# Performance work log

Measured on AMD Instinct MI355X. Metric: run time of the kernel, lower is better.

## Reference

```python
import jax, jax.numpy as jnp
import numpy as np

B, S, D = 1, 2048, 2048
H, G, HD = 32, 8, 64          # heads, kv groups, head_dim
GS = H // G                   # group size = 4
EPS = 1e-6


def _rmsnorm(v, w):
    vf = v.astype(jnp.float32)
    n = vf * jax.lax.rsqrt(jnp.mean(vf * vf, axis=-1, keepdims=True) + EPS)
    return (n * (1.0 + w.astype(jnp.float32))).astype(v.dtype)


def _rope(v, cos, sin):
    # v: [b, h, s, hd]; cos/sin: [s, hd] (rot_dim == head_dim)
    half = v.shape[-1] // 2
    x1, x2 = v[..., :half], v[..., half:]
    rotated = jnp.concatenate([-x2, x1], axis=-1)
    c = cos[None, None, :, :]
    s = sin[None, None, :, :]
    return (v * c + rotated * s).astype(v.dtype)


def setup_inputs() -> dict:
    key = jax.random.key(0)
    ks = jax.random.split(key, 8)
    x = jax.random.normal(ks[0], (B, S, D), dtype=jnp.float32)
    # causal mask: True above diagonal => masked out
    mask = jnp.triu(jnp.ones((S, S), dtype=bool), k=1)
    # standard RoPE tables, full rotary dim == head_dim
    inv_freq = 1.0 / (10000.0 ** (jnp.arange(0, HD, 2, dtype=jnp.float32) / HD))
    angles = jnp.arange(S, dtype=jnp.float32)[:, None] * inv_freq[None, :]
    angles = jnp.concatenate([angles, angles], axis=-1)  # [S, HD]
    cos = jnp.cos(angles)
    sin = jnp.sin(angles)
    sc = 1.0 / np.sqrt(D)
    Wq = jax.random.normal(ks[1], (2 * H * HD, D), dtype=jnp.float32) * sc
    Wk = jax.random.normal(ks[2], (G * HD, D), dtype=jnp.float32) * sc
    Wv = jax.random.normal(ks[3], (G * HD, D), dtype=jnp.float32) * sc
    Wo = jax.random.normal(ks[4], (D, H * HD), dtype=jnp.float32) * sc
    q_norm_w = jnp.zeros((HD,), dtype=jnp.float32)
    k_norm_w = jnp.zeros((HD,), dtype=jnp.float32)
    return {"x": x, "mask": mask, "cos": cos, "sin": sin, "Wq": Wq,
            "Wk": Wk, "Wv": Wv, "Wo": Wo,
            "q_norm_w": q_norm_w, "k_norm_w": k_norm_w}


def reference(x, mask, cos, sin, Wq, Wk, Wv, Wo, q_norm_w, k_norm_w):
    b, s, _ = x.shape
    d_out = H * HD
    # fused q + gate projection: [b, s, H, 2*HD]
    qg = jnp.einsum('bsd,ed->bse', x, Wq).reshape(b, s, H, 2 * HD)
    q = qg[..., :HD]                         # [b, s, H, HD]
    gate = qg[..., HD:].reshape(b, s, d_out)  # [b, s, d_out]
    k = jnp.einsum('bsd,ed->bse', x, Wk).reshape(b, s, G, HD)
    v = jnp.einsum('bsd,ed->bse', x, Wv).reshape(b, s, G, HD)
    q = q.transpose(0, 2, 1, 3)   # [b, H, s, HD]
    k = k.transpose(0, 2, 1, 3)   # [b, G, s, HD]
    v = v.transpose(0, 2, 1, 3)
    q = _rmsnorm(q, q_norm_w)
    k = _rmsnorm(k, k_norm_w)
    q = _rope(q, cos[:s], sin[:s])
    k = _rope(k, cos[:s], sin[:s])
    # GQA without materializing repeated K/V: group queries as [b, G, GS, s, HD]
    qg_ = q.reshape(b, G, GS, s, HD)
    scores = jnp.einsum('bghqd,bgkd->bghqk', qg_, k)   # [b, G, GS, s, s]
    scores = jnp.where(mask[None, None, None, :s, :s], -jnp.inf, scores)
    scale = HD ** (-0.5)
    w = jax.nn.softmax((scores * scale).astype(jnp.float32), axis=-1).astype(q.dtype)
    ctx = jnp.einsum('bghqk,bgkd->bghqd', w, v)        # [b, G, GS, s, HD]
    ctx = ctx.reshape(b, H, s, HD).transpose(0, 2, 1, 3).reshape(b, s, d_out)
    ctx = ctx * jax.nn.sigmoid(gate)
    return jnp.einsum('bse,de->bsd', ctx, Wo)
```

## Files before the change

kernel.cpp:

```cpp
#include <hip/hip_runtime.h>

typedef __bf16 bf16;
typedef __bf16 bf16x4 __attribute__((ext_vector_type(4)));
typedef __bf16 bf16x8 __attribute__((ext_vector_type(8)));
typedef float f32x4 __attribute__((ext_vector_type(4)));

#define DEV static __device__ __forceinline__

constexpr int S  = 2048;
constexpr int D  = 2048;
constexpr int H  = 32;
constexpr int G  = 8;
constexpr int HD = 64;
constexpr int NQG = 2 * H * HD;
constexpr int LDP = 72;

DEV bf16x8 load8(const bf16* p) { return *reinterpret_cast<const bf16x8*>(p); }

DEV f32x4 mfma16(bf16x8 a, bf16x8 b, f32x4 c) {
  return __builtin_amdgcn_mfma_f32_16x16x32_bf16(a, b, c, 0, 0, 0);
}

DEV void gload_lds16(const bf16* g, bf16* l) {
  __builtin_amdgcn_global_load_lds(
      (const __attribute__((address_space(1))) void*)g,
      (__attribute__((address_space(3))) void*)l, 16, 0, 0);
}

#define BARRIER() asm volatile("s_barrier" ::: "memory")
#define VMDRAIN() asm volatile("s_waitcnt vmcnt(0)" ::: "memory")

template <int NISS>
DEV void stage_tile(bf16* lds, const bf16* src_row0, size_t ld, int k0, int tid) {
  const int w = tid >> 6, l = tid & 63;
#pragma unroll
  for (int i = 0; i < NISS; ++i) {
    int blk = w * NISS + i;
    int r = blk * 8 + (l >> 3);
    int c = (l & 7) ^ (r & 7);
    gload_lds16(src_row0 + (size_t)r * ld + k0 + c * 8, lds + blk * 512);
  }
}

DEV void stage64_8w(bf16* lds, const bf16* src_row0, size_t ld, int k0, int tid) {
  const int w = tid >> 6, l = tid & 63;
  int r = w * 8 + (l >> 3);
  int c = (l & 7) ^ (r & 7);
  gload_lds16(src_row0 + (size_t)r * ld + k0 + c * 8, lds + w * 512);
}

DEV bf16x8 fragr(const bf16* T, int row, int chunk) {
  return load8(T + row * 64 + (((chunk ^ (row & 7)) << 3)));
}

DEV float fexp2(float x) { return __builtin_amdgcn_exp2f(x); }
DEV float frcp(float x)  { return __builtin_amdgcn_rcpf(x); }

__global__ __launch_bounds__(256) void cvt_all(
    const float* __restrict__ x,  const float* __restrict__ wq,
    const float* __restrict__ wk, const float* __restrict__ wv,
    const float* __restrict__ wo,
    bf16* __restrict__ xb,  bf16* __restrict__ wqb, bf16* __restrict__ wkb,
    bf16* __restrict__ wvb, bf16* __restrict__ wob)
{
  long c = (long)blockIdx.x * 256 + threadIdx.x;
  const float* src; bf16* dst; long off;
  if      (c <  524288) { src = x;  dst = xb;  off = c; }
  else if (c < 1572864) { src = wq; dst = wqb; off = c -  524288; }
  else if (c < 1703936) { src = wk; dst = wkb; off = c - 1572864; }
  else if (c < 1835008) { src = wv; dst = wvb; off = c - 1703936; }
  else                  { src = wo; dst = wob; off = c - 1835008; }
  long i = off * 8;
  const float4* p = reinterpret_cast<const float4*>(src + i);
  float4 a = p[0], b = p[1];
  bf16x8 o;
  o[0] = (bf16)a.x; o[1] = (bf16)a.y; o[2] = (bf16)a.z; o[3] = (bf16)a.w;
  o[4] = (bf16)b.x; o[5] = (bf16)b.y; o[6] = (bf16)b.z; o[7] = (bf16)b.w;
  *reinterpret_cast<bf16x8*>(dst + i) = o;
}

DEV void rms_rope_store(f32x4 acc[4][4], bf16* __restrict__ dst,
                        const float* __restrict__ w,
                        const float* __restrict__ cosb,
                        const float* __restrict__ sinb,
                        int s0, int ln, int hi, float outscale)
{
  float wgt[4];
#pragma unroll
  for (int ni = 0; ni < 4; ++ni) wgt[ni] = 1.0f + w[ni * 16 + ln];
#pragma unroll
  for (int mi = 0; mi < 4; ++mi)
#pragma unroll
    for (int j = 0; j < 4; ++j) {
      int s = s0 + mi * 16 + hi * 4 + j;
      float v0 = acc[mi][0][j], v1 = acc[mi][1][j];
      float v2 = acc[mi][2][j], v3 = acc[mi][3][j];
      float ss = v0 * v0 + v1 * v1 + v2 * v2 + v3 * v3;
      ss += __shfl_xor(ss, 1);
      ss += __shfl_xor(ss, 2);
      ss += __shfl_xor(ss, 4);
      ss += __shfl_xor(ss, 8);
      float inv = __builtin_amdgcn_rsqf(ss * (1.0f / 64.0f) + 1e-6f);
      float xf[4] = {v0 * inv * wgt[0], v1 * inv * wgt[1],
                     v2 * inv * wgt[2], v3 * inv * wgt[3]};
#pragma unroll
      for (int ni = 0; ni < 4; ++ni) {
        int d = ni * 16 + ln;
        float c  = cosb[s * HD + d];
        float sn = sinb[s * HD + d];
        float rot = (ni < 2) ? -xf[ni + 2] : xf[ni - 2];
        dst[(size_t)s * HD + d] = (bf16)((xf[ni] * c + rot * sn) * outscale);
      }
    }
}

__global__ __launch_bounds__(256, 3) void gemm_qkv(
    const bf16* __restrict__ X, const bf16* __restrict__ Wq,
    const bf16* __restrict__ Wk, const bf16* __restrict__ Wv,
    const float* __restrict__ cosb, const float* __restrict__ sinb,
    const float* __restrict__ qw, const float* __restrict__ kw,
    bf16* __restrict__ qg, bf16* __restrict__ qrot,
    bf16* __restrict__ krot, bf16* __restrict__ vt)
{
  __shared__ __align__(16) bf16 As[128 * 64];
  __shared__ __align__(16) bf16 Bs[128 * 64];

  const int tid  = threadIdx.x;
  const int wave = tid >> 6;
  const int lane = tid & 63;
  const int ln = lane & 15, hi = lane >> 4;
  const int wm = wave >> 1, wn = wave & 1;
  const int m0 = blockIdx.y * 128;
  const int nt = blockIdx.x;

  const bf16* W; int n0;
  if (nt < 32)      { W = Wq; n0 = nt * 128; }
  else if (nt < 36) { W = Wk; n0 = (nt - 32) * 128; }
  else              { W = Wv; n0 = (nt - 36) * 128; }

  const bf16* arow = X + (size_t)m0 * D;
  const bf16* brow = W + (size_t)n0 * D;

  f32x4 acc[4][4] = {};

  for (int k0 = 0; k0 < D; k0 += 64) {
    __syncthreads();
    stage_tile<4>(As, arow, D, k0, tid);
    stage_tile<4>(Bs, brow, D, k0, tid);
    __syncthreads();
#pragma unroll
    for (int kk = 0; kk < 64; kk += 32) {
      bf16x8 a[4], b[4];
#pragma unroll
      for (int mi = 0; mi < 4; ++mi) a[mi] = fragr(As, wm * 64 + mi * 16 + ln, (kk >> 3) + hi);
#pragma unroll
      for (int ni = 0; ni < 4; ++ni) b[ni] = fragr(Bs, wn * 64 + ni * 16 + ln, (kk >> 3) + hi);
#pragma unroll
      for (int mi = 0; mi < 4; ++mi)
#pragma unroll
        for (int ni = 0; ni < 4; ++ni)
          acc[mi][ni] = mfma16(a[mi], b[ni], acc[mi][ni]);
    }
  }

  const int s0 = m0 + wm * 64;
  if (nt < 32) {
    if (wn == 0) {
      rms_rope_store(acc, qrot + (size_t)nt * S * HD, qw, cosb, sinb,
                     s0, ln, hi, 0.18033688011111204f);
    } else {
#pragma unroll
      for (int mi = 0; mi < 4; ++mi)
#pragma unroll
        for (int ni = 0; ni < 4; ++ni)
#pragma unroll
          for (int j = 0; j < 4; ++j) {
            int r = s0 + mi * 16 + hi * 4 + j;
            int c = nt * 128 + 64 + ni * 16 + ln;
            qg[(size_t)r * NQG + c] = (bf16)acc[mi][ni][j];
          }
    }
  } else if (nt < 36) {
    int g8 = (nt - 32) * 2 + wn;
    rms_rope_store(acc, krot + (size_t)g8 * S * HD, kw, cosb, sinb,
                   s0, ln, hi, 1.0f);
  } else {
    int nrel = (nt - 36) * 128;
#pragma unroll
    for (int mi = 0; mi < 4; ++mi)
#pragma unroll
      for (int ni = 0; ni < 4; ++ni)
#pragma unroll
        for (int j = 0; j < 4; ++j) {
          int r = s0 + mi * 16 + hi * 4 + j;
          int c = nrel + wn * 64 + ni * 16 + ln;
          vt[(size_t)c * S + r] = (bf16)acc[mi][ni][j];
        }
  }
}

__global__ __launch_bounds__(256, 3) void gemm_out(
    const bf16* __restrict__ A, const bf16* __restrict__ W,
    float* __restrict__ C)
{
  __shared__ __align__(16) bf16 As[128 * 64];
  __shared__ __align__(16) bf16 Bs[64 * 64];

  const int tid  = threadIdx.x;
  const int wave = tid >> 6;
  const int lane = tid & 63;
  const int ln = lane & 15, hi = lane >> 4;
  const int m0 = blockIdx.y * 128;
  const int n0 = blockIdx.x * 64;

  const bf16* arow = A + (size_t)m0 * D;
  const bf16* brow = W + (size_t)n0 * D;

  f32x4 acc[2][4] = {};

  for (int k0 = 0; k0 < D; k0 += 64) {
    __syncthreads();
    stage_tile<4>(As, arow, D, k0, tid);
    stage_tile<2>(Bs, brow, D, k0, tid);
    __syncthreads();
#pragma unroll
    for (int kk = 0; kk < 64; kk += 32) {
      bf16x8 a[2], b[4];
#pragma unroll
      for (int mi = 0; mi < 2; ++mi) a[mi] = fragr(As, wave * 32 + mi * 16 + ln, (kk >> 3) + hi);
#pragma unroll
      for (int ni = 0; ni < 4; ++ni) b[ni] = fragr(Bs, ni * 16 + ln, (kk >> 3) + hi);
#pragma unroll
      for (int mi = 0; mi < 2; ++mi)
#pragma unroll
        for (int ni = 0; ni < 4; ++ni)
          acc[mi][ni] = mfma16(a[mi], b[ni], acc[mi][ni]);
    }
  }

#pragma unroll
  for (int mi = 0; mi < 2; ++mi)
#pragma unroll
    for (int ni = 0; ni < 4; ++ni)
#pragma unroll
      for (int j = 0; j < 4; ++j) {
        int r = m0 + wave * 32 + mi * 16 + hi * 4 + j;
        int c = n0 + ni * 16 + ln;
        C[(size_t)r * D + c] = acc[mi][ni][j];
      }
}

DEV void attn_phase(const bf16* __restrict__ qrot, const bf16* __restrict__ krow,
                    const bf16* __restrict__ vrow, const bf16* __restrict__ qg,
                    bf16* __restrict__ ctxg,
                    bf16* Kb0, bf16* Kb1, bf16* Vb0, bf16* Vb1, bf16* pw,
                    int h, int qchunk, int nt, int ln, int hi, int tid)
{
  const int qb = qchunk * 64 + ((tid >> 6) & 3) * 16;
  const int q  = qb + ln;

  const bf16* qbase = qrot + ((size_t)h * S + qb + ln) * HD + hi * 8;
  bf16x8 q0 = load8(qbase);
  bf16x8 q1 = load8(qbase + 32);

  f32x4 po[4] = {};
  float m = -INFINITY, l = 0.f;

  stage64_8w(Kb0, krow, 64, 0, tid);
  stage64_8w(Vb0, vrow, S, 0, tid);
  VMDRAIN();
  BARRIER();

  int cur = 0;
  for (int t = 0; t < nt; ++t) {
    const bf16* Kb = cur ? Kb1 : Kb0;
    const bf16* Vb = cur ? Vb1 : Vb0;

    if (t + 1 < nt) {
      bf16* Kn = cur ? Kb0 : Kb1;
      bf16* Vn = cur ? Vb0 : Vb1;
      stage64_8w(Kn, krow + (size_t)(t + 1) * 64 * 64, 64, 0, tid);
      stage64_8w(Vn, vrow, S, (t + 1) * 64, tid);
    }

    bf16x8 kf0[4], kf1[4];
#pragma unroll
    for (int kr = 0; kr < 4; ++kr) {
      kf0[kr] = fragr(Kb, kr * 16 + ln, hi);
      kf1[kr] = fragr(Kb, kr * 16 + ln, hi + 4);
    }
    bf16x8 bv0[4], bv1[4];
#pragma unroll
    for (int dt = 0; dt < 4; ++dt) {
      bv0[dt] = fragr(Vb, dt * 16 + ln, hi);
      bv1[dt] = fragr(Vb, dt * 16 + ln, hi + 4);
    }

    f32x4 sc[4] = {};
    __builtin_amdgcn_s_setprio(1);
#pragma unroll
    for (int kr = 0; kr < 4; ++kr) {
      sc[kr] = mfma16(kf0[kr], q0, sc[kr]);
      sc[kr] = mfma16(kf1[kr], q1, sc[kr]);
    }
    __builtin_amdgcn_s_setprio(0);

    float pmax = -INFINITY;
    if (t == nt - 1) {
      const int key0 = t << 6;
#pragma unroll
      for (int kr = 0; kr < 4; ++kr)
#pragma unroll
        for (int j = 0; j < 4; ++j) {
          int key = key0 + kr * 16 + hi * 4 + j;
          float v = (key <= q) ? sc[kr][j] : -INFINITY;
          sc[kr][j] = v;
          pmax = fmaxf(pmax, v);
        }
    } else {
#pragma unroll
      for (int kr = 0; kr < 4; ++kr)
#pragma unroll
        for (int j = 0; j < 4; ++j) pmax = fmaxf(pmax, sc[kr][j]);
    }
    pmax = fmaxf(pmax, __shfl_xor(pmax, 16));
    pmax = fmaxf(pmax, __shfl_xor(pmax, 32));

    if (__any(pmax > m + 8.0f)) {
      float mn = fmaxf(m, pmax);
      float c  = fexp2(m - mn);
      l *= c;
      float cc[4];
#pragma unroll
      for (int j = 0; j < 4; ++j) cc[j] = __shfl(c, hi * 4 + j);
#pragma unroll
      for (int dt = 0; dt < 4; ++dt)
#pragma unroll
        for (int j = 0; j < 4; ++j) po[dt][j] *= cc[j];
      m = mn;
    }

    float ps = 0.f;
#pragma unroll
    for (int kr = 0; kr < 4; ++kr)
#pragma unroll
      for (int j = 0; j < 4; ++j) {
        float e = fexp2(sc[kr][j] - m);
        sc[kr][j] = e;
        ps += e;
      }
    ps += __shfl_xor(ps, 16);
    ps += __shfl_xor(ps, 32);
    l += ps;

#pragma unroll
    for (int kr = 0; kr < 4; ++kr) {
      unsigned w0, w1;
      asm("v_cvt_pk_bf16_f32 %0, %1, %2" : "=v"(w0) : "v"(sc[kr][0]), "v"(sc[kr][1]));
      asm("v_cvt_pk_bf16_f32 %0, %1, %2" : "=v"(w1) : "v"(sc[kr][2]), "v"(sc[kr][3]));
      uint2 w = {w0, w1};
      *reinterpret_cast<uint2*>(pw + ln * LDP + kr * 16 + hi * 4) = w;
    }
    bf16x8 pa0 = load8(pw + ln * LDP + hi * 8);
    bf16x8 pa1 = load8(pw + ln * LDP + 32 + hi * 8);

    __builtin_amdgcn_s_setprio(1);
#pragma unroll
    for (int dt = 0; dt < 4; ++dt) {
      po[dt] = mfma16(pa0, bv0[dt], po[dt]);
      po[dt] = mfma16(pa1, bv1[dt], po[dt]);
    }
    __builtin_amdgcn_s_setprio(0);

    VMDRAIN();
    BARRIER();
    cur ^= 1;
  }

  float lf[4];
#pragma unroll
  for (int j = 0; j < 4; ++j) lf[j] = __shfl(l, hi * 4 + j);
#pragma unroll
  for (int dt = 0; dt < 4; ++dt)
#pragma unroll
    for (int j = 0; j < 4; ++j) {
      int qq = qb + hi * 4 + j;
      int d  = dt * 16 + ln;
      float o  = po[dt][j] * frcp(lf[j]);
      float gv = (float)qg[(size_t)qq * NQG + h * 128 + 64 + d];
      float sg = frcp(1.0f + fexp2(gv * -1.442695040888963f));
      ctxg[(size_t)qq * D + h * 64 + d] = (bf16)(o * sg);
    }
}

__global__ __launch_bounds__(512) void attn(
    const bf16* __restrict__ qrot, const bf16* __restrict__ krot,
    const bf16* __restrict__ vt, const bf16* __restrict__ qg,
    bf16* __restrict__ ctxg)
{
  __shared__ __align__(16) bf16 Kbuf[2][64 * 64];
  __shared__ __align__(16) bf16 Vbuf[2][64 * 64];
  __shared__ __align__(16) bf16 Pl[8][16 * LDP];

  const int tid  = threadIdx.x;
  const int lane = tid & 63;
  const int ln = lane & 15, hi = lane >> 4;

  const int bid = blockIdx.x;
  const int g   = bid & 7;
  const int i   = bid >> 3;
  const int hp  = i & 1;
  const int pr  = i >> 1;
  const int h   = g * 4 + hp * 2 + ((tid >> 6) >> 2);
  bf16* pw = &Pl[tid >> 6][0];

  const bf16* krow = krot + (size_t)g * S * HD;
  const bf16* vrow = vt + (size_t)g * 64 * S;

  attn_phase(qrot, krow, vrow, qg, ctxg,
             &Kbuf[0][0], &Kbuf[1][0], &Vbuf[0][0], &Vbuf[1][0], pw,
             h, pr, pr + 1, ln, hi, tid);
  attn_phase(qrot, krow, vrow, qg, ctxg,
             &Kbuf[0][0], &Kbuf[1][0], &Vbuf[0][0], &Vbuf[1][0], pw,
             h, 31 - pr, 32 - pr, ln, hi, tid);
}

extern "C" void kernel_launch(void* const* d_in, const int* in_sizes, int n_in,
                              void* d_out, int out_size, void* d_ws, size_t ws_size,
                              hipStream_t stream) {
  const float* x    = (const float*)d_in[0];
  const float* cosb = (const float*)d_in[2];
  const float* sinb = (const float*)d_in[3];
  const float* Wq   = (const float*)d_in[4];
  const float* Wk   = (const float*)d_in[5];
  const float* Wv   = (const float*)d_in[6];
  const float* Wo   = (const float*)d_in[7];
  const float* qw   = (const float*)d_in[8];
  const float* kw   = (const float*)d_in[9];

  char* ws = (char*)d_ws;
  bf16* xb   = (bf16*)(ws);
  bf16* Wqb  = (bf16*)(ws + ( 8u << 20));
  bf16* Wkb  = (bf16*)(ws + (24u << 20));
  bf16* Wvb  = (bf16*)(ws + (26u << 20));
  bf16* Wob  = (bf16*)(ws + (28u << 20));
  bf16* qg   = (bf16*)(ws + (36u << 20));
  bf16* vt   = (bf16*)(ws + (54u << 20));
  bf16* qrot = (bf16*)(ws + (56u << 20));
  bf16* krot = (bf16*)(ws + (64u << 20));
  bf16* ctxg = (bf16*)(ws + (66u << 20));
  float* out = (float*)d_out;

  cvt_all<<<dim3(9216), 256, 0, stream>>>(x, Wq, Wk, Wv, Wo,
                                          xb, Wqb, Wkb, Wvb, Wob);

  gemm_qkv<<<dim3(40, 16), 256, 0, stream>>>(xb, Wqb, Wkb, Wvb,
                                             cosb, sinb, qw, kw,
                                             qg, qrot, krot, vt);
  attn<<<dim3(256), 512, 0, stream>>>(qrot, krot, vt, qg, ctxg);
  gemm_out<<<dim3(32, 16), 256, 0, stream>>>(ctxg, Wob, out);
}
```

Measured before the change: 135.5 us.

## Widen attention KV tiles to 128 keys and fold Wo conversion into QKV GEMM

The attention loop now handles 128 keys per iteration, with double-buffered 2x64 K/V LDS tiles and a wider P staging buffer. This halves the number of barriers and online-softmax rescale steps per query chunk. V fragments are now read from LDS inside the PV MFMA loop instead of being preloaded. Separately, the Wo fp32-to-bf16 conversion moves out of cvt_all into extra blocks of gemm_qkv, so it can overlap with the GEMM. The costs are more LDS and registers per block, and wasted work on the half-masked last tile for even query chunks.

```diff
diff --git a/kernel.cpp b/kernel.cpp
--- a/kernel.cpp
+++ b/kernel.cpp
@@ -13,7 +13,7 @@
 constexpr int G  = 8;
 constexpr int HD = 64;
 constexpr int NQG = 2 * H * HD;
-constexpr int LDP = 72;
+constexpr int LDP = 136;
 
 DEV bf16x8 load8(const bf16* p) { return *reinterpret_cast<const bf16x8*>(p); }
 
@@ -59,17 +59,15 @@
 __global__ __launch_bounds__(256) void cvt_all(
     const float* __restrict__ x,  const float* __restrict__ wq,
     const float* __restrict__ wk, const float* __restrict__ wv,
-    const float* __restrict__ wo,
     bf16* __restrict__ xb,  bf16* __restrict__ wqb, bf16* __restrict__ wkb,
-    bf16* __restrict__ wvb, bf16* __restrict__ wob)
+    bf16* __restrict__ wvb)
 {
   long c = (long)blockIdx.x * 256 + threadIdx.x;
   const float* src; bf16* dst; long off;
   if      (c <  524288) { src = x;  dst = xb;  off = c; }
   else if (c < 1572864) { src = wq; dst = wqb; off = c -  524288; }
   else if (c < 1703936) { src = wk; dst = wkb; off = c - 1572864; }
-  else if (c < 1835008) { src = wv; dst = wvb; off = c - 1703936; }
-  else                  { src = wo; dst = wob; off = c - 1835008; }
+  else                  { src = wv; dst = wvb; off = c - 1703936; }
   long i = off * 8;
   const float4* p = reinterpret_cast<const float4*>(src + i);
   float4 a = p[0], b = p[1];
@@ -119,6 +117,7 @@
     const bf16* __restrict__ Wk, const bf16* __restrict__ Wv,
     const float* __restrict__ cosb, const float* __restrict__ sinb,
     const float* __restrict__ qw, const float* __restrict__ kw,
+    const float* __restrict__ wo, bf16* __restrict__ wob,
     bf16* __restrict__ qg, bf16* __restrict__ qrot,
     bf16* __restrict__ krot, bf16* __restrict__ vt)
 {
@@ -126,12 +125,28 @@
   __shared__ __align__(16) bf16 Bs[128 * 64];
 
   const int tid  = threadIdx.x;
+  const int nt = blockIdx.x;
+
+  if (nt >= 40) {
+    long base = (long)((nt - 40) * 16 + blockIdx.y) * 256 + tid;
+#pragma unroll
+    for (int it = 0; it < 16; ++it) {
+      long i = (base + (long)it * 32768) * 8;
+      const float4* p = reinterpret_cast<const float4*>(wo + i);
+      float4 a = p[0], b = p[1];
+      bf16x8 o;
+      o[0] = (bf16)a.x; o[1] = (bf16)a.y; o[2] = (bf16)a.z; o[3] = (bf16)a.w;
+      o[4] = (bf16)b.x; o[5] = (bf16)b.y; o[6] = (bf16)b.z; o[7] = (bf16)b.w;
+      *reinterpret_cast<bf16x8*>(wob + i) = o;
+    }
+    return;
+  }
+
   const int wave = tid >> 6;
   const int lane = tid & 63;
   const int ln = lane & 15, hi = lane >> 4;
   const int wm = wave >> 1, wn = wave & 1;
   const int m0 = blockIdx.y * 128;
-  const int nt = blockIdx.x;
 
   const bf16* W; int n0;
   if (nt < 32)      { W = Wq; n0 = nt * 128; }
@@ -253,9 +268,10 @@
 DEV void attn_phase(const bf16* __restrict__ qrot, const bf16* __restrict__ krow,
                     const bf16* __restrict__ vrow, const bf16* __restrict__ qg,
                     bf16* __restrict__ ctxg,
-                    bf16* Kb0, bf16* Kb1, bf16* Vb0, bf16* Vb1, bf16* pw,
-                    int h, int qchunk, int nt, int ln, int hi, int tid)
-{
+                    bf16* Kbase, bf16* Vbase, bf16* pw,
+                    int h, int qchunk, int ln, int hi, int tid)
+{
+  const int nt = (qchunk >> 1) + 1;
   const int qb = qchunk * 64 + ((tid >> 6) & 3) * 16;
   const int q  = qb + ln;
 
@@ -266,62 +282,68 @@
   f32x4 po[4] = {};
   float m = -INFINITY, l = 0.f;
 
-  stage64_8w(Kb0, krow, 64, 0, tid);
-  stage64_8w(Vb0, vrow, S, 0, tid);
+  stage64_8w(Kbase,        krow,            64, 0,  tid);
+  stage64_8w(Kbase + 4096, krow + 64 * 64,  64, 0,  tid);
+  stage64_8w(Vbase,        vrow,            S,  0,  tid);
+  stage64_8w(Vbase + 4096, vrow,            S,  64, tid);
   VMDRAIN();
   BARRIER();
 
   int cur = 0;
   for (int t = 0; t < nt; ++t) {
-    const bf16* Kb = cur ? Kb1 : Kb0;
-    const bf16* Vb = cur ? Vb1 : Vb0;
+    const bf16* Kc = Kbase + cur * 8192;
+    const bf16* Vc = Vbase + cur * 8192;
 
     if (t + 1 < nt) {
-      bf16* Kn = cur ? Kb0 : Kb1;
-      bf16* Vn = cur ? Vb0 : Vb1;
-      stage64_8w(Kn, krow + (size_t)(t + 1) * 64 * 64, 64, 0, tid);
-      stage64_8w(Vn, vrow, S, (t + 1) * 64, tid);
-    }
-
-    bf16x8 kf0[4], kf1[4];
-#pragma unroll
-    for (int kr = 0; kr < 4; ++kr) {
-      kf0[kr] = fragr(Kb, kr * 16 + ln, hi);
-      kf1[kr] = fragr(Kb, kr * 16 + ln, hi + 4);
-    }
-    bf16x8 bv0[4], bv1[4];
-#pragma unroll
-    for (int dt = 0; dt < 4; ++dt) {
-      bv0[dt] = fragr(Vb, dt * 16 + ln, hi);
-      bv1[dt] = fragr(Vb, dt * 16 + ln, hi + 4);
-    }
-
-    f32x4 sc[4] = {};
-    __builtin_amdgcn_s_setprio(1);
-#pragma unroll
-    for (int kr = 0; kr < 4; ++kr) {
-      sc[kr] = mfma16(kf0[kr], q0, sc[kr]);
-      sc[kr] = mfma16(kf1[kr], q1, sc[kr]);
-    }
-    __builtin_amdgcn_s_setprio(0);
+      bf16* Kn = Kbase + (cur ^ 1) * 8192;
+      bf16* Vn = Vbase + (cur ^ 1) * 8192;
+      stage64_8w(Kn,        krow + (size_t)(t + 1) * 128 * 64,        64, 0, tid);
+      stage64_8w(Kn + 4096, krow + ((size_t)(t + 1) * 128 + 64) * 64, 64, 0, tid);
+      stage64_8w(Vn,        vrow, S, (t + 1) * 128,      tid);
+      stage64_8w(Vn + 4096, vrow, S, (t + 1) * 128 + 64, tid);
+    }
+
+    f32x4 sc[2][4];
+#pragma unroll
+    for (int s = 0; s < 2; ++s) {
+      const bf16* Ks = Kc + s * 4096;
+      bf16x8 kf0[4], kf1[4];
+#pragma unroll
+      for (int kr = 0; kr < 4; ++kr) {
+        kf0[kr] = fragr(Ks, kr * 16 + ln, hi);
+        kf1[kr] = fragr(Ks, kr * 16 + ln, hi + 4);
+      }
+      __builtin_amdgcn_s_setprio(1);
+#pragma unroll
+      for (int kr = 0; kr < 4; ++kr) {
+        f32x4 z = {};
+        z = mfma16(kf0[kr], q0, z);
+        sc[s][kr] = mfma16(kf1[kr], q1, z);
+      }
+      __builtin_amdgcn_s_setprio(0);
+    }
 
     float pmax = -INFINITY;
     if (t == nt - 1) {
-      const int key0 = t << 6;
-#pragma unroll
-      for (int kr = 0; kr < 4; ++kr)
-#pragma unroll
-        for (int j = 0; j < 4; ++j) {
-          int key = key0 + kr * 16 + hi * 4 + j;
-          float v = (key <= q) ? sc[kr][j] : -INFINITY;
-          sc[kr][j] = v;
-          pmax = fmaxf(pmax, v);
-        }
+      const int key0 = t * 128;
+#pragma unroll
+      for (int s = 0; s < 2; ++s)
+#pragma unroll
+        for (int kr = 0; kr < 4; ++kr)
+#pragma unroll
+          for (int j = 0; j < 4; ++j) {
+            int key = key0 + s * 64 + kr * 16 + hi * 4 + j;
+            float v = (key <= q) ? sc[s][kr][j] : -INFINITY;
+            sc[s][kr][j] = v;
+            pmax = fmaxf(pmax, v);
+          }
     } else {
 #pragma unroll
-      for (int kr = 0; kr < 4; ++kr)
-#pragma unroll
-        for (int j = 0; j < 4; ++j) pmax = fmaxf(pmax, sc[kr][j]);
+      for (int s = 0; s < 2; ++s)
+#pragma unroll
+        for (int kr = 0; kr < 4; ++kr)
+#pragma unroll
+          for (int j = 0; j < 4; ++j) pmax = fmaxf(pmax, sc[s][kr][j]);
     }
     pmax = fmaxf(pmax, __shfl_xor(pmax, 16));
     pmax = fmaxf(pmax, __shfl_xor(pmax, 32));
@@ -342,33 +364,41 @@
 
     float ps = 0.f;
 #pragma unroll
-    for (int kr = 0; kr < 4; ++kr)
-#pragma unroll
-      for (int j = 0; j < 4; ++j) {
-        float e = fexp2(sc[kr][j] - m);
-        sc[kr][j] = e;
-        ps += e;
-      }
+    for (int s = 0; s < 2; ++s)
+#pragma unroll
+      for (int kr = 0; kr < 4; ++kr)
+#pragma unroll
+        for (int j = 0; j < 4; ++j) {
+          float e = fexp2(sc[s][kr][j] - m);
+          sc[s][kr][j] = e;
+          ps += e;
+        }
     ps += __shfl_xor(ps, 16);
     ps += __shfl_xor(ps, 32);
     l += ps;
 
 #pragma unroll
-    for (int kr = 0; kr < 4; ++kr) {
-      unsigned w0, w1;
-      asm("v_cvt_pk_bf16_f32 %0, %1, %2" : "=v"(w0) : "v"(sc[kr][0]), "v"(sc[kr][1]));
-      asm("v_cvt_pk_bf16_f32 %0, %1, %2" : "=v"(w1) : "v"(sc[kr][2]), "v"(sc[kr][3]));
-      uint2 w = {w0, w1};
-      *reinterpret_cast<uint2*>(pw + ln * LDP + kr * 16 + hi * 4) = w;
-    }
-    bf16x8 pa0 = load8(pw + ln * LDP + hi * 8);
-    bf16x8 pa1 = load8(pw + ln * LDP + 32 + hi * 8);
+    for (int s = 0; s < 2; ++s)
+#pragma unroll
+      for (int kr = 0; kr < 4; ++kr) {
+        unsigned w0, w1;
+        asm("v_cvt_pk_bf16_f32 %0, %1, %2" : "=v"(w0) : "v"(sc[s][kr][0]), "v"(sc[s][kr][1]));
+        asm("v_cvt_pk_bf16_f32 %0, %1, %2" : "=v"(w1) : "v"(sc[s][kr][2]), "v"(sc[s][kr][3]));
+        uint2 w = {w0, w1};
+        *reinterpret_cast<uint2*>(pw + ln * LDP + s * 64 + kr * 16 + hi * 4) = w;
+      }
+    bf16x8 pa[4];
+#pragma unroll
+    for (int sl = 0; sl < 4; ++sl) pa[sl] = load8(pw + ln * LDP + sl * 32 + hi * 8);
 
     __builtin_amdgcn_s_setprio(1);
 #pragma unroll
-    for (int dt = 0; dt < 4; ++dt) {
-      po[dt] = mfma16(pa0, bv0[dt], po[dt]);
-      po[dt] = mfma16(pa1, bv1[dt], po[dt]);
+    for (int sl = 0; sl < 4; ++sl) {
+      const bf16* Vs = Vc + (sl >> 1) * 4096;
+      const int ch = (sl & 1) * 4 + hi;
+#pragma unroll
+      for (int dt = 0; dt < 4; ++dt)
+        po[dt] = mfma16(pa[sl], fragr(Vs, dt * 16 + ln, ch), po[dt]);
     }
     __builtin_amdgcn_s_setprio(0);
 
@@ -398,8 +428,8 @@
     const bf16* __restrict__ vt, const bf16* __restrict__ qg,
     bf16* __restrict__ ctxg)
 {
-  __shared__ __align__(16) bf16 Kbuf[2][64 * 64];
-  __shared__ __align__(16) bf16 Vbuf[2][64 * 64];
+  __shared__ __align__(16) bf16 Kbuf[2][2][64 * 64];
+  __shared__ __align__(16) bf16 Vbuf[2][2][64 * 64];
   __shared__ __align__(16) bf16 Pl[8][16 * LDP];
 
   const int tid  = threadIdx.x;
@@ -418,11 +448,9 @@
   const bf16* vrow = vt + (size_t)g * 64 * S;
 
   attn_phase(qrot, krow, vrow, qg, ctxg,
-             &Kbuf[0][0], &Kbuf[1][0], &Vbuf[0][0], &Vbuf[1][0], pw,
-             h, pr, pr + 1, ln, hi, tid);
+             &Kbuf[0][0][0], &Vbuf[0][0][0], pw, h, pr, ln, hi, tid);
   attn_phase(qrot, krow, vrow, qg, ctxg,
-             &Kbuf[0][0], &Kbuf[1][0], &Vbuf[0][0], &Vbuf[1][0], pw,
-             h, 31 - pr, 32 - pr, ln, hi, tid);
+             &Kbuf[0][0][0], &Vbuf[0][0][0], pw, h, 31 - pr, ln, hi, tid);
 }
 
 extern "C" void kernel_launch(void* const* d_in, const int* in_sizes, int n_in,
@@ -451,11 +479,11 @@
   bf16* ctxg = (bf16*)(ws + (66u << 20));
   float* out = (float*)d_out;
 
-  cvt_all<<<dim3(9216), 256, 0, stream>>>(x, Wq, Wk, Wv, Wo,
-                                          xb, Wqb, Wkb, Wvb, Wob);
-
-  gemm_qkv<<<dim3(40, 16), 256, 0, stream>>>(xb, Wqb, Wkb, Wvb,
+  cvt_all<<<dim3(7168), 256, 0, stream>>>(x, Wq, Wk, Wv, xb, Wqb, Wkb, Wvb);
+
+  gemm_qkv<<<dim3(48, 16), 256, 0, stream>>>(xb, Wqb, Wkb, Wvb,
                                              cosb, sinb, qw, kw,
+                                             Wo, Wob,
                                              qg, qrot, krot, vt);
   attn<<<dim3(256), 512, 0, stream>>>(qrot, krot, vt, qg, ctxg);
   gemm_out<<<dim3(32, 16), 256, 0, stream>>>(ctxg, Wob, out);
```

Result: faster. 130.6 us, median of 2 (-3.6%).
